# Kernel optimization log

Measured on AMD Instinct MI355X. Metric: run time of the kernel, lower is better.

The kernel has to match this reference:

```python
import jax, jax.numpy as jnp
import numpy as np

B, S, DM, H, FF = 2, 2048, 1024, 16, 4096
DH = DM // H
EPS = 1e-5


def setup_inputs() -> dict:
    key = jax.random.key(0)
    ks = jax.random.split(key, 16)
    s = 0.02
    return {
        "x": jax.random.normal(ks[0], (B, S, DM), jnp.float32),
        "mask": jnp.ones((B, S), jnp.int32),
        "Wq": jax.random.normal(ks[1], (DM, DM), jnp.float32) * s,
        "bq": jnp.zeros((DM,), jnp.float32),
        "Wk": jax.random.normal(ks[2], (DM, DM), jnp.float32) * s,
        "bk": jnp.zeros((DM,), jnp.float32),
        "Wv": jax.random.normal(ks[3], (DM, DM), jnp.float32) * s,
        "bv": jnp.zeros((DM,), jnp.float32),
        "Wo": jax.random.normal(ks[4], (DM, DM), jnp.float32) * s,
        "bo": jnp.zeros((DM,), jnp.float32),
        "W1": jax.random.normal(ks[5], (DM, FF), jnp.float32) * s,
        "b1": jnp.zeros((FF,), jnp.float32),
        "W2": jax.random.normal(ks[6], (FF, DM), jnp.float32) * s,
        "b2": jnp.zeros((DM,), jnp.float32),
        "g1": jnp.ones((DM,), jnp.float32),
        "beta1": jnp.zeros((DM,), jnp.float32),
        "g2": jnp.ones((DM,), jnp.float32),
        "beta2": jnp.zeros((DM,), jnp.float32),
    }


def _layer_norm(x, g, b):
    mu = jnp.mean(x, axis=-1, keepdims=True)
    var = jnp.var(x, axis=-1, keepdims=True)
    return (x - mu) * jax.lax.rsqrt(var + EPS) * g + b


def reference(x, mask, Wq, bq, Wk, bk, Wv, bv, Wo, bo, W1, b1, W2, b2, g1, beta1, g2, beta2):
    # --- hollow multi-head attention ---
    q = (x @ Wq + bq).reshape(B, S, H, DH)
    k = (x @ Wk + bk).reshape(B, S, H, DH)
    v = (x @ Wv + bv).reshape(B, S, H, DH)
    scores = jnp.einsum("bqhd,bkhd->bhqk", q, k) / jnp.sqrt(jnp.float32(DH))
    # triu(diag=1) and tril(diag=-1) masks kill everything off-diagonal
    diag = jnp.eye(S, dtype=bool)  # [S, S]
    scores = jnp.where(diag[None, None], scores, -jnp.inf)
    attn = jax.nn.softmax(scores, axis=-1)
    out = jnp.einsum("bhqk,bkhd->bqhd", attn, v).reshape(B, S, DM)
    attn_out = out @ Wo + bo
    # --- residual + LN1 ---
    h = _layer_norm(x + attn_out, g1, beta1)
    # --- FFN ---
    ff = jax.nn.relu(h @ W1 + b1) @ W2 + b2
    # --- residual + LN2 ---
    return _layer_norm(h + ff, g2, beta2)
```

## Files before the change

### kernel.cpp

```cpp
#include <hip/hip_runtime.h>
#include <stdint.h>

typedef __bf16 bf16x8 __attribute__((ext_vector_type(8)));
typedef float f32x4 __attribute__((ext_vector_type(4)));

__device__ __forceinline__ uint16_t f2bf(float f) {
  union { float f; uint32_t u; } c; c.f = f;
  uint32_t u = c.u;
  u += 0x7fffu + ((u >> 16) & 1u);
  return (uint16_t)(u >> 16);
}
__device__ __forceinline__ float bf2f(uint16_t u) {
  union { uint32_t u; float f; } c; c.u = (uint32_t)u << 16; return c.f;
}

__device__ __forceinline__ void cvt_body(const float* __restrict__ in,
                                         uint16_t* __restrict__ out, int i) {
  float4 v = reinterpret_cast<const float4*>(in)[i];
  ushort4 o;
  o.x = f2bf(v.x); o.y = f2bf(v.y); o.z = f2bf(v.z); o.w = f2bf(v.w);
  reinterpret_cast<ushort4*>(out)[i] = o;
}

__global__ void prep_kernel(const float* __restrict__ x, const float* __restrict__ Wv,
                            const float* __restrict__ Wo, const float* __restrict__ W1,
                            const float* __restrict__ W2, const float* __restrict__ bv,
                            const float* __restrict__ bo,
                            uint16_t* __restrict__ xb, uint16_t* __restrict__ wvb,
                            uint16_t* __restrict__ woT, uint16_t* __restrict__ w1t,
                            uint16_t* __restrict__ w2t, float* __restrict__ bc) {
  __shared__ float tsh[32][33];
  __shared__ float red[8][32];
  int b = blockIdx.x;
  const int t = threadIdx.x;
  if (b < 4096) { cvt_body(x, xb, b * 256 + t); return; }
  b -= 4096;
  if (b < 1024) { cvt_body(Wv, wvb, b * 256 + t); return; }
  b -= 1024;

  const float* tin = nullptr; uint16_t* tout = nullptr;
  int R = 0, C = 0, bx = 0, by = 0;
  if (b < 1024) {
    tin = Wo; tout = woT; R = 1024; C = 1024; bx = b & 31; by = b >> 5;
  } else if (b < 1024 + 4096) {
    const int bb = b - 1024;
    tin = W1; tout = w1t; R = 1024; C = 4096; bx = bb & 127; by = bb >> 7;
  } else if (b < 1024 + 8192) {
    const int bb = b - (1024 + 4096);
    tin = W2; tout = w2t; R = 4096; C = 1024; bx = bb & 31; by = bb >> 5;
  } else {
    const int jb = b - (1024 + 8192);
    const int jl = t & 31, kg = t >> 5;
    const int j = jb * 32 + jl;
    float s = 0.f;
    const int k0 = kg * 128;
    for (int k = k0; k < k0 + 128; ++k) s += bv[k] * Wo[(size_t)k * 1024 + j];
    red[kg][jl] = s;
    __syncthreads();
    if (kg == 0) {
      float acc = bo[j];
#pragma unroll
      for (int q = 0; q < 8; ++q) acc += red[q][jl];
      bc[j] = acc;
    }
    return;
  }
  const int tx = t & 31, ty = t >> 5;
  const int c0 = bx * 32, r0 = by * 32;
#pragma unroll
  for (int i = 0; i < 4; ++i)
    tsh[ty + i * 8][tx] = tin[(size_t)(r0 + ty + i * 8) * C + (c0 + tx)];
  __syncthreads();
#pragma unroll
  for (int i = 0; i < 4; ++i)
    tout[(size_t)(c0 + ty + i * 8) * R + (r0 + tx)] = f2bf(tsh[tx][ty + i * 8]);
}

constexpr int BM = 128, BN = 128, BK = 64;

template <int MODE>
__launch_bounds__(256, 2)
__global__ void gemm2ph_kernel(const uint16_t* __restrict__ A, const uint16_t* __restrict__ Bt,
                               const float* __restrict__ bias, const float* __restrict__ res,
                               void* __restrict__ out, int M, int N, int Klen, int lda, int ldb) {
  __shared__ uint16_t sAB[2][2][BM * BK];
  const int tid  = threadIdx.x;
  const int lane = tid & 63;
  const int wave = tid >> 6;

  const int nwg = gridDim.x * gridDim.y;
  int wg = blockIdx.y * gridDim.x + blockIdx.x;
  wg = (wg & 7) * (nwg >> 3) + (wg >> 3);
  const int bx = wg % gridDim.x, by = wg / gridDim.x;
  const int m0 = by * BM, n0 = bx * BN;

  const int wm = (wave >> 1) * 64;
  const int wn = (wave & 1) * 64;

  f32x4 acc[4][4] = {};

  const int srow = tid >> 3;
  const int scol = ((tid & 7) ^ (srow & 7)) * 8;
  const uint16_t* ga[4];
  const uint16_t* gb[4];
  uint32_t loff[4];
#pragma unroll
  for (int g = 0; g < 4; ++g) {
    const int row = srow + 32 * g;
    ga[g] = A + (size_t)(m0 + row) * lda + scol;
    gb[g] = Bt + (size_t)(n0 + row) * ldb + scol;
    loff[g] = (uint32_t)(tid + g * 256) * 8;
  }

  const int fr = lane & 15;
  const int hi = lane >> 4;
  const int rx = fr & 7;

  const int nk = Klen / BK;

#define STAGE2(buf, kt)                                                                   \
  {                                                                                       \
    _Pragma("unroll")                                                                     \
    for (int g = 0; g < 4; ++g) {                                                         \
      __builtin_amdgcn_global_load_lds(                                                   \
          (const __attribute__((address_space(1))) uint32_t*)(ga[g] + (size_t)(kt) * BK), \
          (__attribute__((address_space(3))) uint32_t*)(&sAB[buf][0][loff[g]]), 16, 0, 0);\
      __builtin_amdgcn_global_load_lds(                                                   \
          (const __attribute__((address_space(1))) uint32_t*)(gb[g] + (size_t)(kt) * BK), \
          (__attribute__((address_space(3))) uint32_t*)(&sAB[buf][1][loff[g]]), 16, 0, 0);\
    }                                                                                     \
  }

  STAGE2(0, 0);
  __syncthreads();

  int cur = 0;
  for (int kt = 0; kt < nk; ++kt) {
    if (kt + 1 < nk) STAGE2(cur ^ 1, kt + 1);
    const uint16_t* pA = &sAB[cur][0][0];
    const uint16_t* pB = &sAB[cur][1][0];
    bf16x8 af[4][2], bb[4][2];
#pragma unroll
    for (int m = 0; m < 4; ++m)
#pragma unroll
      for (int ks = 0; ks < 2; ++ks) {
        const int slot = (ks * 4 + hi) ^ rx;
        af[m][ks] = *reinterpret_cast<const bf16x8*>(pA + (wm + m * 16 + fr) * BK + slot * 8);
        bb[m][ks] = *reinterpret_cast<const bf16x8*>(pB + (wn + m * 16 + fr) * BK + slot * 8);
      }
#pragma unroll
    for (int ks = 0; ks < 2; ++ks)
#pragma unroll
      for (int m = 0; m < 4; ++m)
#pragma unroll
        for (int n = 0; n < 4; ++n)
          acc[m][n] = __builtin_amdgcn_mfma_f32_16x16x32_bf16(af[m][ks], bb[n][ks], acc[m][n], 0, 0, 0);
    __syncthreads();
    cur ^= 1;
  }
#undef STAGE2

  const int cn  = lane & 15;
  const int cm4 = (lane >> 4) * 4;
#pragma unroll
  for (int m = 0; m < 4; ++m) {
#pragma unroll
    for (int n = 0; n < 4; ++n) {
      const int gm = m0 + wm + m * 16 + cm4;
      const int gn = n0 + wn + n * 16 + cn;
      const float bbv = bias ? bias[gn] : 0.f;
#pragma unroll
      for (int r = 0; r < 4; ++r) {
        const size_t idx = (size_t)(gm + r) * N + gn;
        const float vv = acc[m][n][r] + bbv;
        if constexpr (MODE == 0) {
          ((uint16_t*)out)[idx] = f2bf(vv);
        } else {
          ((float*)out)[idx] = vv + res[idx];
        }
      }
    }
  }
}

template <int MODE>
__launch_bounds__(512, 2)
__global__ void gemm8ph_kernel(const uint16_t* __restrict__ A, const uint16_t* __restrict__ Bt,
                               const float* __restrict__ bias, void* __restrict__ out,
                               int M, int N, int Klen, int lda, int ldb) {
  extern __shared__ uint16_t lds[];
  const int tid  = threadIdx.x;
  const int lane = tid & 63;
  const int wave = tid >> 6;

  const int nwg = gridDim.x * gridDim.y;
  int wg = blockIdx.y * gridDim.x + blockIdx.x;
  wg = (wg & 7) * (nwg >> 3) + (wg >> 3);
  const int bx = wg % gridDim.x, by = wg / gridDim.x;
  const int m0 = by * 256, n0 = bx * 256;

  const int z = blockIdx.z;
  A  += (size_t)z * Klen;
  Bt += (size_t)z * Klen;

  const int wm = (wave >> 2) * 128;
  const int wn = (wave & 3) * 64;

  f32x4 acc[8][4] = {};

  const int srw = tid >> 3;
  const int sp  = tid & 7;
  const uint16_t* gu[8];
#pragma unroll
  for (int u = 0; u < 8; ++u) {
    const int key = (srw ^ (srw >> 3) ^ u) & 7;
    const uint16_t* base = (u < 4) ? A + (size_t)(m0 + u * 64) * lda
                                   : Bt + (size_t)(n0 + (u - 4) * 64) * ldb;
    const int ld = (u < 4) ? lda : ldb;
    gu[u] = base + (size_t)srw * ld + ((sp ^ key) * 8);
  }

  const int nk = Klen / 64;

#define STAGE8(T, U)                                                                          \
  if ((T) < nk) {                                                                             \
    __builtin_amdgcn_global_load_lds(                                                         \
        (const __attribute__((address_space(1))) uint32_t*)(gu[U] + (size_t)(T) * 64),        \
        (__attribute__((address_space(3))) uint32_t*)(lds + ((T) & 1) * 32768 + (U) * 4096 +  \
                                                      tid * 8),                               \
        16, 0, 0);                                                                            \
  }

  const int fr = lane & 15;
  const int hi = lane >> 4;
  int aoff[8];
#pragma unroll
  for (int m = 0; m < 8; ++m) {
    const int u = (wm >> 6) + (m >> 2);
    const int R = (m & 3) * 16 + fr;
    const int key = (R ^ (R >> 3) ^ u) & 7;
    aoff[m] = u * 4096 + R * 64 + ((hi ^ key) * 8);
  }
  int boff[4];
#pragma unroll
  for (int n = 0; n < 4; ++n) {
    const int u = 4 + (wn >> 6);
    const int R = n * 16 + fr;
    const int key = (R ^ (R >> 3) ^ u) & 7;
    boff[n] = u * 4096 + R * 64 + ((hi ^ key) * 8);
  }

  STAGE8(0, 0); STAGE8(0, 2); STAGE8(0, 1); STAGE8(0, 3);
  STAGE8(0, 4); STAGE8(0, 5); STAGE8(0, 6); STAGE8(0, 7);
  STAGE8(1, 4); STAGE8(1, 5); STAGE8(1, 6); STAGE8(1, 7);
  asm volatile("s_waitcnt vmcnt(4)" ::: "memory");
  __builtin_amdgcn_s_barrier();

#define LD8(off) (*reinterpret_cast<const bf16x8*>(bufp + (off)))
#define PHASE_MFMA(q)                                                         \
  __builtin_amdgcn_s_setprio(1);                                              \
  _Pragma("unroll") for (int ks = 0; ks < 2; ++ks)                            \
    _Pragma("unroll") for (int mm = 0; mm < 2; ++mm)                          \
      _Pragma("unroll") for (int n = 0; n < 4; ++n)                           \
        acc[2 * (q) + mm][n] = __builtin_amdgcn_mfma_f32_16x16x32_bf16(       \
            aq[mm][ks], bq[n][ks], acc[2 * (q) + mm][n], 0, 0, 0);            \
  __builtin_amdgcn_s_setprio(0);

  for (int k = 0; k < nk; ++k) {
    const uint16_t* bufp = lds + (k & 1) * 32768;
    bf16x8 bq[4][2], aq[2][2];
#pragma unroll
    for (int n = 0; n < 4; ++n) { bq[n][0] = LD8(boff[n]); bq[n][1] = LD8(boff[n] ^ 32); }
#pragma unroll
    for (int mm = 0; mm < 2; ++mm) { aq[mm][0] = LD8(aoff[mm]); aq[mm][1] = LD8(aoff[mm] ^ 32); }
    STAGE8(k + 1, 0); STAGE8(k + 1, 2);
    __builtin_amdgcn_s_barrier();
    asm volatile("s_waitcnt lgkmcnt(0)" ::: "memory");
    __builtin_amdgcn_sched_barrier(0);
    PHASE_MFMA(0);
    __builtin_amdgcn_s_barrier();
#pragma unroll
    for (int mm = 0; mm < 2; ++mm) { aq[mm][0] = LD8(aoff[2 + mm]); aq[mm][1] = LD8(aoff[2 + mm] ^ 32); }
    STAGE8(k + 1, 1); STAGE8(k + 1, 3);
    if (k < nk - 1) { asm volatile("s_waitcnt vmcnt(8)" ::: "memory"); }
    else            { asm volatile("s_waitcnt vmcnt(0)" ::: "memory"); }
    __builtin_amdgcn_s_barrier();
    asm volatile("s_waitcnt lgkmcnt(0)" ::: "memory");
    __builtin_amdgcn_sched_barrier(0);
    PHASE_MFMA(1);
    __builtin_amdgcn_s_barrier();
#pragma unroll
    for (int mm = 0; mm < 2; ++mm) { aq[mm][0] = LD8(aoff[4 + mm]); aq[mm][1] = LD8(aoff[4 + mm] ^ 32); }
    STAGE8(k + 2, 4); STAGE8(k + 2, 5);
    __builtin_amdgcn_s_barrier();
    asm volatile("s_waitcnt lgkmcnt(0)" ::: "memory");
    __builtin_amdgcn_sched_barrier(0);
    PHASE_MFMA(2);
    __builtin_amdgcn_s_barrier();
#pragma unroll
    for (int mm = 0; mm < 2; ++mm) { aq[mm][0] = LD8(aoff[6 + mm]); aq[mm][1] = LD8(aoff[6 + mm] ^ 32); }
    STAGE8(k + 2, 6); STAGE8(k + 2, 7);
    if (k < nk - 2)      { asm volatile("s_waitcnt vmcnt(6)" ::: "memory"); }
    else if (k == nk - 2){ asm volatile("s_waitcnt vmcnt(2)" ::: "memory"); }
    else                 { asm volatile("s_waitcnt vmcnt(0)" ::: "memory"); }
    __builtin_amdgcn_s_barrier();
    asm volatile("s_waitcnt lgkmcnt(0)" ::: "memory");
    __builtin_amdgcn_sched_barrier(0);
    PHASE_MFMA(3);
    __builtin_amdgcn_s_barrier();
  }
#undef PHASE_MFMA
#undef LD8
#undef STAGE8

  const int cn  = lane & 15;
  const int cm4 = (lane >> 4) * 4;
  uint16_t* outp = (uint16_t*)out;
  if constexpr (MODE == 1) outp += (size_t)z * M * N;
  float bias_n[4];
  if constexpr (MODE == 0) {
#pragma unroll
    for (int n = 0; n < 4; ++n) bias_n[n] = bias[n0 + wn + n * 16 + cn];
  }
#pragma unroll
  for (int m = 0; m < 8; ++m) {
#pragma unroll
    for (int n = 0; n < 4; ++n) {
      const int gm = m0 + wm + m * 16 + cm4;
      const int gn = n0 + wn + n * 16 + cn;
#pragma unroll
      for (int r = 0; r < 4; ++r) {
        const size_t idx = (size_t)(gm + r) * N + gn;
        if constexpr (MODE == 0) {
          outp[idx] = f2bf(fmaxf(acc[m][n][r] + bias_n[n], 0.f));
        } else {
          outp[idx] = f2bf(acc[m][n][r]);
        }
      }
    }
  }
}

__global__ void ln1_kernel(const float* __restrict__ in,
                           const float* __restrict__ g,
                           const float* __restrict__ b,
                           uint16_t* __restrict__ outb) {
  const int row = blockIdx.x;
  const int t = threadIdx.x;
  const float4 v = reinterpret_cast<const float4*>(in + (size_t)row * 1024)[t];
  float s  = v.x + v.y + v.z + v.w;
  float s2 = v.x * v.x + v.y * v.y + v.z * v.z + v.w * v.w;
#pragma unroll
  for (int o = 32; o > 0; o >>= 1) { s += __shfl_down(s, o); s2 += __shfl_down(s2, o); }
  __shared__ float red[8];
  const int lane = t & 63, wave = t >> 6;
  if (lane == 0) { red[wave] = s; red[4 + wave] = s2; }
  __syncthreads();
  const float S  = red[0] + red[1] + red[2] + red[3];
  const float S2 = red[4] + red[5] + red[6] + red[7];
  const float mu  = S * (1.f / 1024.f);
  const float var = S2 * (1.f / 1024.f) - mu * mu;
  const float rs  = rsqrtf(var + 1e-5f);
  const float4 gg = reinterpret_cast<const float4*>(g)[t];
  const float4 bb = reinterpret_cast<const float4*>(b)[t];
  ushort4 ob;
  ob.x = f2bf((v.x - mu) * rs * gg.x + bb.x);
  ob.y = f2bf((v.y - mu) * rs * gg.y + bb.y);
  ob.z = f2bf((v.z - mu) * rs * gg.z + bb.z);
  ob.w = f2bf((v.w - mu) * rs * gg.w + bb.w);
  reinterpret_cast<ushort4*>(outb + (size_t)row * 1024)[t] = ob;
}

__global__ void ln2_kernel(const uint16_t* __restrict__ pp, size_t pstride,
                           const uint16_t* __restrict__ hb, const float* __restrict__ b2,
                           const float* __restrict__ g, const float* __restrict__ be,
                           float* __restrict__ out) {
  const int row = blockIdx.x;
  const int t = threadIdx.x;
  const size_t base = (size_t)row * 1024;
  const ushort4 h4 = reinterpret_cast<const ushort4*>(hb + base)[t];
  const float4 c2 = reinterpret_cast<const float4*>(b2)[t];
  float4 v;
  v.x = c2.x + bf2f(h4.x); v.y = c2.y + bf2f(h4.y);
  v.z = c2.z + bf2f(h4.z); v.w = c2.w + bf2f(h4.w);
#pragma unroll
  for (int zz = 0; zz < 4; ++zz) {
    const ushort4 p4 = reinterpret_cast<const ushort4*>(pp + zz * pstride + base)[t];
    v.x += bf2f(p4.x); v.y += bf2f(p4.y); v.z += bf2f(p4.z); v.w += bf2f(p4.w);
  }
  float s  = v.x + v.y + v.z + v.w;
  float s2 = v.x * v.x + v.y * v.y + v.z * v.z + v.w * v.w;
#pragma unroll
  for (int o = 32; o > 0; o >>= 1) { s += __shfl_down(s, o); s2 += __shfl_down(s2, o); }
  __shared__ float red[8];
  const int lane = t & 63, wave = t >> 6;
  if (lane == 0) { red[wave] = s; red[4 + wave] = s2; }
  __syncthreads();
  const float S  = red[0] + red[1] + red[2] + red[3];
  const float S2 = red[4] + red[5] + red[6] + red[7];
  const float mu  = S * (1.f / 1024.f);
  const float var = S2 * (1.f / 1024.f) - mu * mu;
  const float rs  = rsqrtf(var + 1e-5f);
  const float4 gg = reinterpret_cast<const float4*>(g)[t];
  const float4 bb = reinterpret_cast<const float4*>(be)[t];
  float4 o;
  o.x = (v.x - mu) * rs * gg.x + bb.x;
  o.y = (v.y - mu) * rs * gg.y + bb.y;
  o.z = (v.z - mu) * rs * gg.z + bb.z;
  o.w = (v.w - mu) * rs * gg.w + bb.w;
  reinterpret_cast<float4*>(out + base)[t] = o;
}

extern "C" void kernel_launch(void* const* d_in, const int* in_sizes, int n_in,
                              void* d_out, int out_size, void* d_ws, size_t ws_size,
                              hipStream_t stream) {
  const float* x   = (const float*)d_in[0];
  const float* Wv  = (const float*)d_in[6];
  const float* bv  = (const float*)d_in[7];
  const float* Wo  = (const float*)d_in[8];
  const float* bo  = (const float*)d_in[9];
  const float* W1  = (const float*)d_in[10];
  const float* b1  = (const float*)d_in[11];
  const float* W2  = (const float*)d_in[12];
  const float* b2  = (const float*)d_in[13];
  const float* g1  = (const float*)d_in[14];
  const float* be1 = (const float*)d_in[15];
  const float* g2  = (const float*)d_in[16];
  const float* be2 = (const float*)d_in[17];
  float* out = (float*)d_out;

  constexpr int M = 4096, DM = 1024, FF = 4096;

  char* p = (char*)d_ws;
  auto alloc = [&](size_t bytes) {
    char* r = p;
    p += (bytes + 255) & ~(size_t)255;
    return r;
  };
  uint16_t* xb  = (uint16_t*)alloc((size_t)M * DM * 2);
  uint16_t* wvb = (uint16_t*)alloc((size_t)DM * DM * 2);
  uint16_t* woT = (uint16_t*)alloc((size_t)DM * DM * 2);
  uint16_t* w1t = (uint16_t*)alloc((size_t)FF * DM * 2);
  uint16_t* w2t = (uint16_t*)alloc((size_t)DM * FF * 2);
  uint16_t* wcT = (uint16_t*)alloc((size_t)DM * DM * 2);
  float*    bc  = (float*)   alloc((size_t)DM * 4);
  float*    r1  = (float*)   alloc((size_t)M * DM * 4);
  uint16_t* hb  = (uint16_t*)alloc((size_t)M * DM * 2);
  uint16_t* tb  = (uint16_t*)alloc((size_t)M * FF * 2);
  uint16_t* pp  = (uint16_t*)alloc((size_t)4 * M * DM * 2);

  (void)hipFuncSetAttribute(reinterpret_cast<const void*>(gemm8ph_kernel<0>),
                            hipFuncAttributeMaxDynamicSharedMemorySize, 131072);
  (void)hipFuncSetAttribute(reinterpret_cast<const void*>(gemm8ph_kernel<1>),
                            hipFuncAttributeMaxDynamicSharedMemorySize, 131072);

  prep_kernel<<<4096 + 1024 + 1024 + 4096 + 4096 + 32, 256, 0, stream>>>(
      x, Wv, Wo, W1, W2, bv, bo, xb, wvb, woT, w1t, w2t, bc);

  gemm2ph_kernel<0><<<dim3(DM / BN, DM / BM), 256, 0, stream>>>(
      woT, wvb, nullptr, nullptr, wcT, DM, DM, DM, DM, DM);
  gemm2ph_kernel<1><<<dim3(DM / BN, M / BM), 256, 0, stream>>>(
      xb, wcT, bc, x, r1, M, DM, DM, DM, DM);
  ln1_kernel<<<M, 256, 0, stream>>>(r1, g1, be1, hb);
  gemm8ph_kernel<0><<<dim3(FF / 256, M / 256), 512, 131072, stream>>>(
      hb, w1t, b1, tb, M, FF, DM, DM, DM);
  gemm8ph_kernel<1><<<dim3(DM / 256, M / 256, 4), 512, 131072, stream>>>(
      tb, w2t, nullptr, pp, M, DM, FF / 4, FF, FF);
  ln2_kernel<<<M, 256, 0, stream>>>(pp, (size_t)M * DM, hb, b2, g2, be2, out);
}
```

Baseline: 156.1 us.

## Store residual as bf16, simplify LDS swizzle, reorder MFMA phases by K-half

The residual output of the attention projection GEMM is now written as bf16 instead of fp32, and LN1 reads bf16, which halves that intermediate's traffic at some precision cost. The LDS XOR swizzle key is simplified to row&7. The 8-phase GEMM inner loop now processes K-halves separately with four A fragments per phase instead of two A fragments times two K-steps. The loop change alters register use and the MFMA/LDS-load interleaving.

```diff
diff --git a/kernel.cpp b/kernel.cpp
--- a/kernel.cpp
+++ b/kernel.cpp
@@ -176,7 +176,7 @@
         if constexpr (MODE == 0) {
           ((uint16_t*)out)[idx] = f2bf(vv);
         } else {
-          ((float*)out)[idx] = vv + res[idx];
+          ((uint16_t*)out)[idx] = f2bf(vv + res[idx]);
         }
       }
     }
@@ -213,11 +213,10 @@
   const uint16_t* gu[8];
 #pragma unroll
   for (int u = 0; u < 8; ++u) {
-    const int key = (srw ^ (srw >> 3) ^ u) & 7;
     const uint16_t* base = (u < 4) ? A + (size_t)(m0 + u * 64) * lda
                                    : Bt + (size_t)(n0 + (u - 4) * 64) * ldb;
     const int ld = (u < 4) ? lda : ldb;
-    gu[u] = base + (size_t)srw * ld + ((sp ^ key) * 8);
+    gu[u] = base + (size_t)srw * ld + ((sp ^ (srw & 7)) * 8);
   }
 
   const int nk = Klen / 64;
@@ -238,16 +237,14 @@
   for (int m = 0; m < 8; ++m) {
     const int u = (wm >> 6) + (m >> 2);
     const int R = (m & 3) * 16 + fr;
-    const int key = (R ^ (R >> 3) ^ u) & 7;
-    aoff[m] = u * 4096 + R * 64 + ((hi ^ key) * 8);
+    aoff[m] = u * 4096 + R * 64 + ((hi ^ (R & 7)) * 8);
   }
   int boff[4];
 #pragma unroll
   for (int n = 0; n < 4; ++n) {
     const int u = 4 + (wn >> 6);
     const int R = n * 16 + fr;
-    const int key = (R ^ (R >> 3) ^ u) & 7;
-    boff[n] = u * 4096 + R * 64 + ((hi ^ key) * 8);
+    boff[n] = u * 4096 + R * 64 + ((hi ^ (R & 7)) * 8);
   }
 
   STAGE8(0, 0); STAGE8(0, 2); STAGE8(0, 1); STAGE8(0, 3);
@@ -257,22 +254,21 @@
   __builtin_amdgcn_s_barrier();
 
 #define LD8(off) (*reinterpret_cast<const bf16x8*>(bufp + (off)))
-#define PHASE_MFMA(q)                                                         \
+#define PHASE_MFMA(MB)                                                        \
   __builtin_amdgcn_s_setprio(1);                                              \
-  _Pragma("unroll") for (int ks = 0; ks < 2; ++ks)                            \
-    _Pragma("unroll") for (int mm = 0; mm < 2; ++mm)                          \
-      _Pragma("unroll") for (int n = 0; n < 4; ++n)                           \
-        acc[2 * (q) + mm][n] = __builtin_amdgcn_mfma_f32_16x16x32_bf16(       \
-            aq[mm][ks], bq[n][ks], acc[2 * (q) + mm][n], 0, 0, 0);            \
+  _Pragma("unroll") for (int mm = 0; mm < 4; ++mm)                            \
+    _Pragma("unroll") for (int n = 0; n < 4; ++n)                             \
+      acc[(MB) + mm][n] = __builtin_amdgcn_mfma_f32_16x16x32_bf16(            \
+          aq[mm], bq[n], acc[(MB) + mm][n], 0, 0, 0);                         \
   __builtin_amdgcn_s_setprio(0);
 
   for (int k = 0; k < nk; ++k) {
     const uint16_t* bufp = lds + (k & 1) * 32768;
-    bf16x8 bq[4][2], aq[2][2];
-#pragma unroll
-    for (int n = 0; n < 4; ++n) { bq[n][0] = LD8(boff[n]); bq[n][1] = LD8(boff[n] ^ 32); }
-#pragma unroll
-    for (int mm = 0; mm < 2; ++mm) { aq[mm][0] = LD8(aoff[mm]); aq[mm][1] = LD8(aoff[mm] ^ 32); }
+    bf16x8 bq[4], aq[4];
+#pragma unroll
+    for (int n = 0; n < 4; ++n) bq[n] = LD8(boff[n]);
+#pragma unroll
+    for (int mm = 0; mm < 4; ++mm) aq[mm] = LD8(aoff[mm]);
     STAGE8(k + 1, 0); STAGE8(k + 1, 2);
     __builtin_amdgcn_s_barrier();
     asm volatile("s_waitcnt lgkmcnt(0)" ::: "memory");
@@ -280,25 +276,27 @@
     PHASE_MFMA(0);
     __builtin_amdgcn_s_barrier();
 #pragma unroll
-    for (int mm = 0; mm < 2; ++mm) { aq[mm][0] = LD8(aoff[2 + mm]); aq[mm][1] = LD8(aoff[2 + mm] ^ 32); }
+    for (int mm = 0; mm < 4; ++mm) aq[mm] = LD8(aoff[4 + mm]);
     STAGE8(k + 1, 1); STAGE8(k + 1, 3);
     if (k < nk - 1) { asm volatile("s_waitcnt vmcnt(8)" ::: "memory"); }
     else            { asm volatile("s_waitcnt vmcnt(0)" ::: "memory"); }
     __builtin_amdgcn_s_barrier();
     asm volatile("s_waitcnt lgkmcnt(0)" ::: "memory");
     __builtin_amdgcn_sched_barrier(0);
-    PHASE_MFMA(1);
-    __builtin_amdgcn_s_barrier();
-#pragma unroll
-    for (int mm = 0; mm < 2; ++mm) { aq[mm][0] = LD8(aoff[4 + mm]); aq[mm][1] = LD8(aoff[4 + mm] ^ 32); }
+    PHASE_MFMA(4);
+    __builtin_amdgcn_s_barrier();
+#pragma unroll
+    for (int n = 0; n < 4; ++n) bq[n] = LD8(boff[n] ^ 32);
+#pragma unroll
+    for (int mm = 0; mm < 4; ++mm) aq[mm] = LD8(aoff[mm] ^ 32);
     STAGE8(k + 2, 4); STAGE8(k + 2, 5);
     __builtin_amdgcn_s_barrier();
     asm volatile("s_waitcnt lgkmcnt(0)" ::: "memory");
     __builtin_amdgcn_sched_barrier(0);
-    PHASE_MFMA(2);
-    __builtin_amdgcn_s_barrier();
-#pragma unroll
-    for (int mm = 0; mm < 2; ++mm) { aq[mm][0] = LD8(aoff[6 + mm]); aq[mm][1] = LD8(aoff[6 + mm] ^ 32); }
+    PHASE_MFMA(0);
+    __builtin_amdgcn_s_barrier();
+#pragma unroll
+    for (int mm = 0; mm < 4; ++mm) aq[mm] = LD8(aoff[4 + mm] ^ 32);
     STAGE8(k + 2, 6); STAGE8(k + 2, 7);
     if (k < nk - 2)      { asm volatile("s_waitcnt vmcnt(6)" ::: "memory"); }
     else if (k == nk - 2){ asm volatile("s_waitcnt vmcnt(2)" ::: "memory"); }
@@ -306,7 +304,7 @@
     __builtin_amdgcn_s_barrier();
     asm volatile("s_waitcnt lgkmcnt(0)" ::: "memory");
     __builtin_amdgcn_sched_barrier(0);
-    PHASE_MFMA(3);
+    PHASE_MFMA(4);
     __builtin_amdgcn_s_barrier();
   }
 #undef PHASE_MFMA
@@ -341,13 +339,15 @@
   }
 }
 
-__global__ void ln1_kernel(const float* __restrict__ in,
+__global__ void ln1_kernel(const uint16_t* __restrict__ in,
                            const float* __restrict__ g,
                            const float* __restrict__ b,
                            uint16_t* __restrict__ outb) {
   const int row = blockIdx.x;
   const int t = threadIdx.x;
-  const float4 v = reinterpret_cast<const float4*>(in + (size_t)row * 1024)[t];
+  const ushort4 r4 = reinterpret_cast<const ushort4*>(in + (size_t)row * 1024)[t];
+  float4 v;
+  v.x = bf2f(r4.x); v.y = bf2f(r4.y); v.z = bf2f(r4.z); v.w = bf2f(r4.w);
   float s  = v.x + v.y + v.z + v.w;
   float s2 = v.x * v.x + v.y * v.y + v.z * v.z + v.w * v.w;
 #pragma unroll
@@ -444,7 +444,7 @@
   uint16_t* w2t = (uint16_t*)alloc((size_t)DM * FF * 2);
   uint16_t* wcT = (uint16_t*)alloc((size_t)DM * DM * 2);
   float*    bc  = (float*)   alloc((size_t)DM * 4);
-  float*    r1  = (float*)   alloc((size_t)M * DM * 4);
+  uint16_t* r1b = (uint16_t*)alloc((size_t)M * DM * 2);
   uint16_t* hb  = (uint16_t*)alloc((size_t)M * DM * 2);
   uint16_t* tb  = (uint16_t*)alloc((size_t)M * FF * 2);
   uint16_t* pp  = (uint16_t*)alloc((size_t)4 * M * DM * 2);
@@ -460,8 +460,8 @@
   gemm2ph_kernel<0><<<dim3(DM / BN, DM / BM), 256, 0, stream>>>(
       woT, wvb, nullptr, nullptr, wcT, DM, DM, DM, DM, DM);
   gemm2ph_kernel<1><<<dim3(DM / BN, M / BM), 256, 0, stream>>>(
-      xb, wcT, bc, x, r1, M, DM, DM, DM, DM);
-  ln1_kernel<<<M, 256, 0, stream>>>(r1, g1, be1, hb);
+      xb, wcT, bc, x, r1b, M, DM, DM, DM, DM);
+  ln1_kernel<<<M, 256, 0, stream>>>(r1b, g1, be1, hb);
   gemm8ph_kernel<0><<<dim3(FF / 256, M / 256), 512, 131072, stream>>>(
       hb, w1t, b1, tb, M, FF, DM, DM, DM);
   gemm8ph_kernel<1><<<dim3(DM / 256, M / 256, 4), 512, 131072, stream>>>(
```

New measurement: 147.5 us. 1.06x faster.
